# Kernel optimization log

Hardware: AMD Instinct MI355X
Metric: run time of the kernel (lower is better)

The kernel has to match this reference:

```python
import jax, jax.numpy as jnp
import numpy as np

N_NODES = 65536
N_EDGES = 1048576
IN_F = 128
HID_F = 128
OUT_F = 128


def setup_inputs() -> dict:
    key = jax.random.key(0)
    ks = jax.random.split(key, 8)
    feat = jax.random.normal(ks[0], (N_NODES, IN_F), dtype=jnp.float32)
    eweight = jax.random.uniform(ks[1], (N_EDGES, 1), dtype=jnp.float32)
    W1 = jax.random.normal(ks[2], (IN_F, HID_F), dtype=jnp.float32) * (1.0 / np.sqrt(IN_F))
    b1 = jnp.zeros((HID_F,), dtype=jnp.float32)
    W2 = jax.random.normal(ks[3], (HID_F, OUT_F), dtype=jnp.float32) * (1.0 / np.sqrt(HID_F))
    b2 = jnp.zeros((OUT_F,), dtype=jnp.float32)
    src = jax.random.randint(ks[4], (N_EDGES,), 0, N_NODES, dtype=jnp.int32)
    dst = jax.random.randint(ks[5], (N_EDGES,), 0, N_NODES, dtype=jnp.int32)
    return {"feat": feat, "eweight": eweight, "W1": W1, "b1": b1,
            "W2": W2, "b2": b2, "src": src, "dst": dst}


def _degrees(src, dst, n_nodes):
    ones = jnp.ones(src.shape[0], dtype=jnp.float32)
    deg_out = jax.ops.segment_sum(ones, src, num_segments=n_nodes)
    deg_in = jax.ops.segment_sum(ones, dst, num_segments=n_nodes)
    # DGL GraphConv clamps degree to min 1 before norm='both'
    return jnp.clip(deg_out, 1.0, None), jnp.clip(deg_in, 1.0, None)


def _graph_conv(feat, W, b, src, dst, out_norm, in_norm, n_nodes):
    # DGL GraphConv, norm='both': D_out^{-1/2} x -> x W -> spmm sum -> D_in^{-1/2} -> + b
    h = feat * out_norm[:, None]
    h = h @ W
    agg = jax.ops.segment_sum(h[src], dst, num_segments=n_nodes)
    return agg * in_norm[:, None] + b


def reference(feat, eweight, W1, b1, W2, b2, src, dst):
    n = feat.shape[0]
    deg_out, deg_in = _degrees(src, dst, n)
    out_norm = jax.lax.rsqrt(deg_out)
    in_norm = jax.lax.rsqrt(deg_in)
    h = _graph_conv(feat, W1, b1, src, dst, out_norm, in_norm, n)
    h = jax.nn.relu(h)
    h = _graph_conv(h, W2, b2, src, dst, out_norm, in_norm, n)
    # final update_all: u_mul_e + sum (eweight given)
    msg = h[src] * eweight  # [E, OUT_F]
    return jax.ops.segment_sum(msg, dst, num_segments=n)
```

## Files before the change

kernel.cpp:

```cpp
#include <hip/hip_runtime.h>

#define F 128
#define NBA 512
#define NBS 128
#define COARSE 256
#define CAP_BIN 4864
#define CAP_CSR 5632

typedef unsigned int uint;
typedef unsigned short ushort;
typedef unsigned char uchar;
typedef __attribute__((ext_vector_type(8))) short short8;
typedef __attribute__((ext_vector_type(8))) unsigned short ushort8;
typedef __attribute__((ext_vector_type(4))) float floatx4;

__device__ __forceinline__ ushort f2bf(float f) {
  uint u = __float_as_uint(f);
  u += 0x7fffu + ((u >> 16) & 1u);
  return (ushort)(u >> 16);
}

__global__ __launch_bounds__(256) void w_prep(const float* __restrict__ W1,
                                              const float* __restrict__ W2,
                                              ushort* __restrict__ W1t,
                                              ushort* __restrict__ W2t) {
  int b = blockIdx.x;
  const float* W = (b < 64) ? W1 : W2;
  ushort* Wt = (b < 64) ? W1t : W2t;
  int idx = (b & 63) * 256 + threadIdx.x;
  int k = idx >> 7, n = idx & 127;
  Wt[n * F + k] = f2bf(W[idx]);
}

__global__ __launch_bounds__(256) void bin_edges(
    const int* __restrict__ src, const int* __restrict__ dst,
    const float* __restrict__ ew, int E,
    int* __restrict__ cursorD, int* __restrict__ cursorS,
    uint2* __restrict__ slotD, uchar* __restrict__ srcF) {
  __shared__ int cnt[4][COARSE];
  __shared__ int base[COARSE];
  bool isD = blockIdx.x < NBA;
  int blk = isD ? blockIdx.x : blockIdx.x - NBA;
  int nblk = isD ? NBA : NBS;
  const int* key = isD ? dst : src;
  int* cursor = isD ? cursorD : cursorS;
  int wave = threadIdx.x >> 6;
  for (int i = threadIdx.x; i < 4 * COARSE; i += 256) ((int*)cnt)[i] = 0;
  __syncthreads();
  int chunk = (E + nblk - 1) / nblk;
  int s0 = blk * chunk, s1 = min(E, s0 + chunk);
  for (int i = s0 + threadIdx.x; i < s1; i += 256)
    atomicAdd(&cnt[wave][key[i] >> 8], 1);
  __syncthreads();
  if (threadIdx.x < COARSE) {
    int b = threadIdx.x;
    int tot = cnt[0][b] + cnt[1][b] + cnt[2][b] + cnt[3][b];
    base[b] = tot ? atomicAdd(&cursor[b], tot) : 0;
    cnt[0][b] = 0;
  }
  __syncthreads();
  if (isD) {
    for (int i = s0 + threadIdx.x; i < s1; i += 256) {
      int d = dst[i];
      int bin = d >> 8;
      int p = base[bin] + atomicAdd(&cnt[0][bin], 1);
      if (p < CAP_BIN) {
        uint2 v;
        v.x = (uint)(src[i] & 0xffff) | ((uint)f2bf(ew[i]) << 16);
        v.y = (uint)(d & 255);
        slotD[(size_t)bin * CAP_BIN + p] = v;
      }
    }
  } else {
    for (int i = s0 + threadIdx.x; i < s1; i += 256) {
      int s = src[i];
      int bin = s >> 8;
      int p = base[bin] + atomicAdd(&cnt[0][bin], 1);
      if (p < CAP_BIN) srcF[(size_t)bin * CAP_BIN + p] = (uchar)(s & 255);
    }
  }
}

__global__ __launch_bounds__(1024) void bucket_csr(
    const uint2* __restrict__ slotD, const int* __restrict__ cursorD,
    int2* __restrict__ rowRange, float* __restrict__ inNorm, uint* __restrict__ csr,
    const uchar* __restrict__ srcF, const int* __restrict__ cursorS,
    float* __restrict__ outNorm) {
  __shared__ int hist[256], base[256], cur[256];
  int t = threadIdx.x;
  if (blockIdx.x >= COARSE) {
    int b = blockIdx.x - COARSE;
    int lo = b * CAP_BIN;
    int cntS = min(cursorS[b], CAP_BIN);
    if (t < 256) hist[t] = 0;
    __syncthreads();
    for (int i = lo + t; i < lo + cntS; i += 1024)
      atomicAdd(&hist[srcF[i]], 1);
    __syncthreads();
    if (t < 256) outNorm[b * 256 + t] = rsqrtf((float)max(hist[t], 1));
    return;
  }
  int b = blockIdx.x;
  int lo = b * CAP_BIN;
  int cntD = min(cursorD[b], CAP_BIN);
  int hi = lo + cntD;
  if (t < 256) hist[t] = 0;
  __syncthreads();
  for (int i = lo + t; i < hi; i += 1024)
    atomicAdd(&hist[slotD[i].y], 1);
  __syncthreads();
  if (t < 256) base[t] = (hist[t] + 3) & ~3;
  __syncthreads();
  for (int off = 1; off < 256; off <<= 1) {
    int x = 0;
    if (t < 256 && t >= off) x = base[t - off];
    __syncthreads();
    if (t < 256) base[t] += x;
    __syncthreads();
  }
  if (t < 256) {
    int v = hist[t];
    int sz4 = (v + 3) & ~3;
    int st = b * CAP_CSR + base[t] - sz4;
    base[t] = st;
    cur[t] = 0;
    int node = b * 256 + t;
    rowRange[node] = make_int2(st, v);
    inNorm[node] = rsqrtf((float)max(v, 1));
  }
  __syncthreads();
  for (int i = lo + t; i < hi; i += 1024) {
    uint2 v = slotD[i];
    int fine = v.y;
    int p = base[fine] + atomicAdd(&cur[fine], 1);
    csr[p] = v.x;
  }
}


template <bool BF16IN>
__global__ __launch_bounds__(256) void gemm_mfma(
    const void* __restrict__ Xv, const float* __restrict__ scale,
    const ushort* __restrict__ Wt, ushort* __restrict__ Y) {
  __shared__ ushort sA[128 * 136];
  __shared__ ushort sB[128 * 136];
  int t = threadIdx.x;
  int row0 = blockIdx.x * 128;

  {
    int r = t >> 1, hf = t & 1;
    ushort* ap = sA + r * 136 + hf * 64;
    if (BF16IN) {
      const ushort* xp = (const ushort*)Xv + (size_t)(row0 + r) * F + hf * 64;
#pragma unroll
      for (int j = 0; j < 8; ++j)
        *(ushort8*)(ap + j * 8) = *(const ushort8*)(xp + j * 8);
    } else {
      const float* xp = (const float*)Xv + (size_t)(row0 + r) * F + hf * 64;
      float s = scale[row0 + r];
#pragma unroll
      for (int j = 0; j < 8; ++j) {
        float4 v0 = *(const float4*)(xp + j * 8);
        float4 v1 = *(const float4*)(xp + j * 8 + 4);
        ushort8 o;
        o[0] = f2bf(v0.x * s); o[1] = f2bf(v0.y * s); o[2] = f2bf(v0.z * s); o[3] = f2bf(v0.w * s);
        o[4] = f2bf(v1.x * s); o[5] = f2bf(v1.y * s); o[6] = f2bf(v1.z * s); o[7] = f2bf(v1.w * s);
        *(ushort8*)(ap + j * 8) = o;
      }
    }
  }
  {
    int n = t >> 1, hf = t & 1;
    const ushort* wp = Wt + n * F + hf * 64;
    ushort* bp = sB + n * 136 + hf * 64;
#pragma unroll
    for (int j = 0; j < 8; ++j)
      *(ushort8*)(bp + j * 8) = *(const ushort8*)(wp + j * 8);
  }
  __syncthreads();

  int lane = t & 63, wave = t >> 6;
  int quad = lane >> 4, l16 = lane & 15;
  int mrow0 = wave * 32;

  floatx4 acc[2][8];
#pragma unroll
  for (int a = 0; a < 2; ++a)
#pragma unroll
    for (int c = 0; c < 8; ++c) acc[a][c] = (floatx4){0.f, 0.f, 0.f, 0.f};

#pragma unroll
  for (int kc = 0; kc < 128; kc += 32) {
    short8 afrag[2], bfrag[8];
#pragma unroll
    for (int a = 0; a < 2; ++a)
      afrag[a] = *(const short8*)(sA + (mrow0 + a * 16 + l16) * 136 + kc + quad * 8);
#pragma unroll
    for (int c = 0; c < 8; ++c)
      bfrag[c] = *(const short8*)(sB + (c * 16 + l16) * 136 + kc + quad * 8);
#pragma unroll
    for (int a = 0; a < 2; ++a)
#pragma unroll
      for (int c = 0; c < 8; ++c)
        acc[a][c] = __builtin_amdgcn_mfma_f32_16x16x32_bf16(afrag[a], bfrag[c], acc[a][c], 0, 0, 0);
  }

#pragma unroll
  for (int a = 0; a < 2; ++a)
#pragma unroll
    for (int c = 0; c < 8; ++c)
#pragma unroll
      for (int r = 0; r < 4; ++r) {
        int row = row0 + mrow0 + a * 16 + quad * 4 + r;
        int col = c * 16 + l16;
        Y[(size_t)row * F + col] = f2bf(acc[a][c][r]);
      }
}


template <bool EW, bool NB, bool RELU, bool PS, bool OUT_BF16>
__global__ __launch_bounds__(256) void spmm(
    const ushort* __restrict__ hb, const int2* __restrict__ rowRange,
    const uint* __restrict__ csr, const float* __restrict__ inNorm,
    const float* __restrict__ bias, const float* __restrict__ postScale,
    void* __restrict__ outv) {
  int node = blockIdx.x * 4 + (threadIdx.x >> 6);
  int lane = threadIdx.x & 63;
  int2 rr = rowRange[node];
  int base = rr.x, len = rr.y;

  float ax0 = 0.f, ay0 = 0.f, ax1 = 0.f, ay1 = 0.f;
  float ax2 = 0.f, ay2 = 0.f, ax3 = 0.f, ay3 = 0.f;
  int i = 0;
  for (; i + 8 <= len; i += 8) {
    uint4 c0 = *(const uint4*)(csr + base + i);
    uint4 c1 = *(const uint4*)(csr + base + i + 4);
    uint e0 = c0.x, e1 = c0.y, e2 = c0.z, e3 = c0.w;
    uint e4 = c1.x, e5 = c1.y, e6 = c1.z, e7 = c1.w;
    uint w0 = *((const uint*)(hb + ((size_t)(e0 & 0xffffu) << 7)) + lane);
    uint w1 = *((const uint*)(hb + ((size_t)(e1 & 0xffffu) << 7)) + lane);
    uint w2 = *((const uint*)(hb + ((size_t)(e2 & 0xffffu) << 7)) + lane);
    uint w3 = *((const uint*)(hb + ((size_t)(e3 & 0xffffu) << 7)) + lane);
    uint w4 = *((const uint*)(hb + ((size_t)(e4 & 0xffffu) << 7)) + lane);
    uint w5 = *((const uint*)(hb + ((size_t)(e5 & 0xffffu) << 7)) + lane);
    uint w6 = *((const uint*)(hb + ((size_t)(e6 & 0xffffu) << 7)) + lane);
    uint w7 = *((const uint*)(hb + ((size_t)(e7 & 0xffffu) << 7)) + lane);
    if (EW) {
      float q0 = __uint_as_float(e0 & 0xffff0000u), q1 = __uint_as_float(e1 & 0xffff0000u);
      float q2 = __uint_as_float(e2 & 0xffff0000u), q3 = __uint_as_float(e3 & 0xffff0000u);
      float q4 = __uint_as_float(e4 & 0xffff0000u), q5 = __uint_as_float(e5 & 0xffff0000u);
      float q6 = __uint_as_float(e6 & 0xffff0000u), q7 = __uint_as_float(e7 & 0xffff0000u);
      ax0 = fmaf(__uint_as_float(w0 << 16), q0, ax0); ay0 = fmaf(__uint_as_float(w0 & 0xffff0000u), q0, ay0);
      ax1 = fmaf(__uint_as_float(w1 << 16), q1, ax1); ay1 = fmaf(__uint_as_float(w1 & 0xffff0000u), q1, ay1);
      ax2 = fmaf(__uint_as_float(w2 << 16), q2, ax2); ay2 = fmaf(__uint_as_float(w2 & 0xffff0000u), q2, ay2);
      ax3 = fmaf(__uint_as_float(w3 << 16), q3, ax3); ay3 = fmaf(__uint_as_float(w3 & 0xffff0000u), q3, ay3);
      ax0 = fmaf(__uint_as_float(w4 << 16), q4, ax0); ay0 = fmaf(__uint_as_float(w4 & 0xffff0000u), q4, ay0);
      ax1 = fmaf(__uint_as_float(w5 << 16), q5, ax1); ay1 = fmaf(__uint_as_float(w5 & 0xffff0000u), q5, ay1);
      ax2 = fmaf(__uint_as_float(w6 << 16), q6, ax2); ay2 = fmaf(__uint_as_float(w6 & 0xffff0000u), q6, ay2);
      ax3 = fmaf(__uint_as_float(w7 << 16), q7, ax3); ay3 = fmaf(__uint_as_float(w7 & 0xffff0000u), q7, ay3);
    } else {
      ax0 += __uint_as_float(w0 << 16) + __uint_as_float(w4 << 16);
      ay0 += __uint_as_float(w0 & 0xffff0000u) + __uint_as_float(w4 & 0xffff0000u);
      ax1 += __uint_as_float(w1 << 16) + __uint_as_float(w5 << 16);
      ay1 += __uint_as_float(w1 & 0xffff0000u) + __uint_as_float(w5 & 0xffff0000u);
      ax2 += __uint_as_float(w2 << 16) + __uint_as_float(w6 << 16);
      ay2 += __uint_as_float(w2 & 0xffff0000u) + __uint_as_float(w6 & 0xffff0000u);
      ax3 += __uint_as_float(w3 << 16) + __uint_as_float(w7 << 16);
      ay3 += __uint_as_float(w3 & 0xffff0000u) + __uint_as_float(w7 & 0xffff0000u);
    }
  }
  if (i + 4 <= len) {
    uint4 c = *(const uint4*)(csr + base + i);
    uint e0 = c.x, e1 = c.y, e2 = c.z, e3 = c.w;
    uint w0 = *((const uint*)(hb + ((size_t)(e0 & 0xffffu) << 7)) + lane);
    uint w1 = *((const uint*)(hb + ((size_t)(e1 & 0xffffu) << 7)) + lane);
    uint w2 = *((const uint*)(hb + ((size_t)(e2 & 0xffffu) << 7)) + lane);
    uint w3 = *((const uint*)(hb + ((size_t)(e3 & 0xffffu) << 7)) + lane);
    float q0 = EW ? __uint_as_float(e0 & 0xffff0000u) : 1.f;
    float q1 = EW ? __uint_as_float(e1 & 0xffff0000u) : 1.f;
    float q2 = EW ? __uint_as_float(e2 & 0xffff0000u) : 1.f;
    float q3 = EW ? __uint_as_float(e3 & 0xffff0000u) : 1.f;
    ax0 = fmaf(__uint_as_float(w0 << 16), q0, ax0); ay0 = fmaf(__uint_as_float(w0 & 0xffff0000u), q0, ay0);
    ax1 = fmaf(__uint_as_float(w1 << 16), q1, ax1); ay1 = fmaf(__uint_as_float(w1 & 0xffff0000u), q1, ay1);
    ax2 = fmaf(__uint_as_float(w2 << 16), q2, ax2); ay2 = fmaf(__uint_as_float(w2 & 0xffff0000u), q2, ay2);
    ax3 = fmaf(__uint_as_float(w3 << 16), q3, ax3); ay3 = fmaf(__uint_as_float(w3 & 0xffff0000u), q3, ay3);
    i += 4;
  }
  int r = len - i;
  if (r > 0) {
    uint4 c = *(const uint4*)(csr + base + i);
    uint ee[4] = {c.x, c.y, c.z, c.w};
#pragma unroll
    for (int j = 0; j < 3; ++j) {
      if (j < r) {
        uint wj = *((const uint*)(hb + ((size_t)(ee[j] & 0xffffu) << 7)) + lane);
        float q = EW ? __uint_as_float(ee[j] & 0xffff0000u) : 1.f;
        if (j == 0) { ax0 = fmaf(__uint_as_float(wj << 16), q, ax0); ay0 = fmaf(__uint_as_float(wj & 0xffff0000u), q, ay0); }
        if (j == 1) { ax1 = fmaf(__uint_as_float(wj << 16), q, ax1); ay1 = fmaf(__uint_as_float(wj & 0xffff0000u), q, ay1); }
        if (j == 2) { ax2 = fmaf(__uint_as_float(wj << 16), q, ax2); ay2 = fmaf(__uint_as_float(wj & 0xffff0000u), q, ay2); }
      }
    }
  }
  float rx = (ax0 + ax1) + (ax2 + ax3);
  float ry = (ay0 + ay1) + (ay2 + ay3);
  if (NB) {
    float sc = inNorm[node];
    float2 b = *((const float2*)bias + lane);
    rx = fmaf(rx, sc, b.x);
    ry = fmaf(ry, sc, b.y);
    if (RELU) { rx = fmaxf(rx, 0.f); ry = fmaxf(ry, 0.f); }
    if (PS) { float o = postScale[node]; rx *= o; ry *= o; }
  }
  if (OUT_BF16) {
    uint p = ((uint)f2bf(ry) << 16) | (uint)f2bf(rx);
    *((uint*)outv + ((size_t)node << 6) + lane) = p;
  } else {
    float2 rv = {rx, ry};
    *((float2*)outv + ((size_t)node << 6) + lane) = rv;
  }
}


extern "C" void kernel_launch(void* const* d_in, const int* in_sizes, int n_in,
                              void* d_out, int out_size, void* d_ws, size_t ws_size,
                              hipStream_t stream) {
  const float* feat = (const float*)d_in[0];
  const float* ew   = (const float*)d_in[1];
  const float* W1   = (const float*)d_in[2];
  const float* b1   = (const float*)d_in[3];
  const float* W2   = (const float*)d_in[4];
  const float* b2   = (const float*)d_in[5];
  const int*   src  = (const int*)d_in[6];
  const int*   dst  = (const int*)d_in[7];
  const int N = in_sizes[0] / F;
  const int E = in_sizes[6];
  float* out = (float*)d_out;

  char* ws = (char*)d_ws;
  size_t off = 0;
  auto alloc = [&](size_t bytes) {
    void* p = ws + off;
    off += (bytes + 255) & ~(size_t)255;
    return p;
  };
  int2*   rowRange = (int2*)alloc((size_t)N * 8);
  float*  inNorm   = (float*)alloc((size_t)N * 4);
  float*  outNorm  = (float*)alloc((size_t)N * 4);
  ushort* W1t      = (ushort*)alloc((size_t)F * F * 2);
  ushort* W2t      = (ushort*)alloc((size_t)F * F * 2);
  int*    cursorD  = (int*)alloc(COARSE * 4);
  int*    cursorS  = (int*)alloc(COARSE * 4);
  uint*   csr      = (uint*)alloc((size_t)COARSE * CAP_CSR * 4);
  ushort* bufAb    = (ushort*)alloc((size_t)N * F * 2);
  ushort* bufBb    = (ushort*)alloc((size_t)N * F * 2);
  ushort* bufCb    = (ushort*)alloc((size_t)N * F * 2);
  if (off > ws_size) return;

  uint2* slotD;
  uchar* srcF;
  {
    char* tp = (char*)bufBb;
    size_t toff = 0;
    auto talloc = [&](size_t bytes) {
      void* p = tp + toff;
      toff += (bytes + 255) & ~(size_t)255;
      return p;
    };
    slotD = (uint2*)talloc((size_t)COARSE * CAP_BIN * 8);
    srcF  = (uchar*)talloc((size_t)COARSE * CAP_BIN);
  }

  hipMemsetAsync(cursorD, 0, 2 * COARSE * 4, stream);
  w_prep<<<128, 256, 0, stream>>>(W1, W2, W1t, W2t);
  bin_edges<<<NBA + NBS, 256, 0, stream>>>(src, dst, ew, E, cursorD, cursorS, slotD, srcF);
  bucket_csr<<<2 * COARSE, 1024, 0, stream>>>(slotD, cursorD, rowRange, inNorm, csr,
                                              srcF, cursorS, outNorm);

  gemm_mfma<false><<<N / 128, 256, 0, stream>>>(feat, outNorm, W1t, bufAb);
  spmm<false, true, true, true, true><<<N / 4, 256, 0, stream>>>(
      bufAb, rowRange, csr, inNorm, b1, outNorm, bufBb);
  gemm_mfma<true><<<N / 128, 256, 0, stream>>>(bufBb, nullptr, W2t, bufAb);
  spmm<false, true, false, false, true><<<N / 4, 256, 0, stream>>>(
      bufAb, rowRange, csr, inNorm, b2, nullptr, bufCb);
  spmm<true, false, false, false, false><<<N / 4, 256, 0, stream>>>(
      bufCb, rowRange, csr, nullptr, nullptr, nullptr, out);
}
```

Measured before the change: 281.8 us.

## Split SpMM wave into half-waves gathering two edges with 8-byte loads

The SpMM kernel now has each half of a 64-lane wave gather a different neighbor row. Each lane loads 8 bytes (four bf16 features), and the two halves are combined with a cross-half shuffle before the epilogue. This halves the number of gather load instructions per edge and widens each memory access, at the cost of a shuffle reduction and only half the lanes doing the stores. Separately, the binning kernel now keeps a per-wave prefix offset per bin so scatter atomics are spread over four shared counters instead of one, which reduces LDS atomic contention.

```diff
diff --git a/kernel.cpp b/kernel.cpp
--- a/kernel.cpp
+++ b/kernel.cpp
@@ -38,7 +38,6 @@
     int* __restrict__ cursorD, int* __restrict__ cursorS,
     uint2* __restrict__ slotD, uchar* __restrict__ srcF) {
   __shared__ int cnt[4][COARSE];
-  __shared__ int base[COARSE];
   bool isD = blockIdx.x < NBA;
   int blk = isD ? blockIdx.x : blockIdx.x - NBA;
   int nblk = isD ? NBA : NBS;
@@ -54,16 +53,20 @@
   __syncthreads();
   if (threadIdx.x < COARSE) {
     int b = threadIdx.x;
-    int tot = cnt[0][b] + cnt[1][b] + cnt[2][b] + cnt[3][b];
-    base[b] = tot ? atomicAdd(&cursor[b], tot) : 0;
-    cnt[0][b] = 0;
+    int c0 = cnt[0][b], c1 = cnt[1][b], c2 = cnt[2][b], c3 = cnt[3][b];
+    int tot = c0 + c1 + c2 + c3;
+    int base = tot ? atomicAdd(&cursor[b], tot) : 0;
+    cnt[0][b] = base;
+    cnt[1][b] = base + c0;
+    cnt[2][b] = base + c0 + c1;
+    cnt[3][b] = base + c0 + c1 + c2;
   }
   __syncthreads();
   if (isD) {
     for (int i = s0 + threadIdx.x; i < s1; i += 256) {
       int d = dst[i];
       int bin = d >> 8;
-      int p = base[bin] + atomicAdd(&cnt[0][bin], 1);
+      int p = atomicAdd(&cnt[wave][bin], 1);
       if (p < CAP_BIN) {
         uint2 v;
         v.x = (uint)(src[i] & 0xffff) | ((uint)f2bf(ew[i]) << 16);
@@ -75,7 +78,7 @@
     for (int i = s0 + threadIdx.x; i < s1; i += 256) {
       int s = src[i];
       int bin = s >> 8;
-      int p = base[bin] + atomicAdd(&cnt[0][bin], 1);
+      int p = atomicAdd(&cnt[wave][bin], 1);
       if (p < CAP_BIN) srcF[(size_t)bin * CAP_BIN + p] = (uchar)(s & 255);
     }
   }
@@ -137,7 +140,6 @@
   }
 }
 
-
 template <bool BF16IN>
 __global__ __launch_bounds__(256) void gemm_mfma(
     const void* __restrict__ Xv, const float* __restrict__ scale,
@@ -226,97 +228,95 @@
     void* __restrict__ outv) {
   int node = blockIdx.x * 4 + (threadIdx.x >> 6);
   int lane = threadIdx.x & 63;
+  int half = lane >> 5;
+  int l32 = lane & 31;
   int2 rr = rowRange[node];
   int base = rr.x, len = rr.y;
 
-  float ax0 = 0.f, ay0 = 0.f, ax1 = 0.f, ay1 = 0.f;
-  float ax2 = 0.f, ay2 = 0.f, ax3 = 0.f, ay3 = 0.f;
+  float a0 = 0.f, a1 = 0.f, a2 = 0.f, a3 = 0.f;
+  float b0 = 0.f, b1v = 0.f, b2v = 0.f, b3 = 0.f;
+
+#define PAIR(elo, ehi, A0, A1, A2, A3)                                          \
+  {                                                                             \
+    uint es = half ? (ehi) : (elo);                                             \
+    uint2 w = *(const uint2*)(hb + ((size_t)(es & 0xffffu) << 7) + l32 * 4);    \
+    float q = EW ? __uint_as_float(es & 0xffff0000u) : 1.f;                     \
+    A0 = fmaf(__uint_as_float(w.x << 16), q, A0);                               \
+    A1 = fmaf(__uint_as_float(w.x & 0xffff0000u), q, A1);                       \
+    A2 = fmaf(__uint_as_float(w.y << 16), q, A2);                               \
+    A3 = fmaf(__uint_as_float(w.y & 0xffff0000u), q, A3);                       \
+  }
+
   int i = 0;
   for (; i + 8 <= len; i += 8) {
     uint4 c0 = *(const uint4*)(csr + base + i);
     uint4 c1 = *(const uint4*)(csr + base + i + 4);
-    uint e0 = c0.x, e1 = c0.y, e2 = c0.z, e3 = c0.w;
-    uint e4 = c1.x, e5 = c1.y, e6 = c1.z, e7 = c1.w;
-    uint w0 = *((const uint*)(hb + ((size_t)(e0 & 0xffffu) << 7)) + lane);
-    uint w1 = *((const uint*)(hb + ((size_t)(e1 & 0xffffu) << 7)) + lane);
-    uint w2 = *((const uint*)(hb + ((size_t)(e2 & 0xffffu) << 7)) + lane);
-    uint w3 = *((const uint*)(hb + ((size_t)(e3 & 0xffffu) << 7)) + lane);
-    uint w4 = *((const uint*)(hb + ((size_t)(e4 & 0xffffu) << 7)) + lane);
-    uint w5 = *((const uint*)(hb + ((size_t)(e5 & 0xffffu) << 7)) + lane);
-    uint w6 = *((const uint*)(hb + ((size_t)(e6 & 0xffffu) << 7)) + lane);
-    uint w7 = *((const uint*)(hb + ((size_t)(e7 & 0xffffu) << 7)) + lane);
-    if (EW) {
-      float q0 = __uint_as_float(e0 & 0xffff0000u), q1 = __uint_as_float(e1 & 0xffff0000u);
-      float q2 = __uint_as_float(e2 & 0xffff0000u), q3 = __uint_as_float(e3 & 0xffff0000u);
-      float q4 = __uint_as_float(e4 & 0xffff0000u), q5 = __uint_as_float(e5 & 0xffff0000u);
-      float q6 = __uint_as_float(e6 & 0xffff0000u), q7 = __uint_as_float(e7 & 0xffff0000u);
-      ax0 = fmaf(__uint_as_float(w0 << 16), q0, ax0); ay0 = fmaf(__uint_as_float(w0 & 0xffff0000u), q0, ay0);
-      ax1 = fmaf(__uint_as_float(w1 << 16), q1, ax1); ay1 = fmaf(__uint_as_float(w1 & 0xffff0000u), q1, ay1);
-      ax2 = fmaf(__uint_as_float(w2 << 16), q2, ax2); ay2 = fmaf(__uint_as_float(w2 & 0xffff0000u), q2, ay2);
-      ax3 = fmaf(__uint_as_float(w3 << 16), q3, ax3); ay3 = fmaf(__uint_as_float(w3 & 0xffff0000u), q3, ay3);
-      ax0 = fmaf(__uint_as_float(w4 << 16), q4, ax0); ay0 = fmaf(__uint_as_float(w4 & 0xffff0000u), q4, ay0);
-      ax1 = fmaf(__uint_as_float(w5 << 16), q5, ax1); ay1 = fmaf(__uint_as_float(w5 & 0xffff0000u), q5, ay1);
-      ax2 = fmaf(__uint_as_float(w6 << 16), q6, ax2); ay2 = fmaf(__uint_as_float(w6 & 0xffff0000u), q6, ay2);
-      ax3 = fmaf(__uint_as_float(w7 << 16), q7, ax3); ay3 = fmaf(__uint_as_float(w7 & 0xffff0000u), q7, ay3);
-    } else {
-      ax0 += __uint_as_float(w0 << 16) + __uint_as_float(w4 << 16);
-      ay0 += __uint_as_float(w0 & 0xffff0000u) + __uint_as_float(w4 & 0xffff0000u);
-      ax1 += __uint_as_float(w1 << 16) + __uint_as_float(w5 << 16);
-      ay1 += __uint_as_float(w1 & 0xffff0000u) + __uint_as_float(w5 & 0xffff0000u);
-      ax2 += __uint_as_float(w2 << 16) + __uint_as_float(w6 << 16);
-      ay2 += __uint_as_float(w2 & 0xffff0000u) + __uint_as_float(w6 & 0xffff0000u);
-      ax3 += __uint_as_float(w3 << 16) + __uint_as_float(w7 << 16);
-      ay3 += __uint_as_float(w3 & 0xffff0000u) + __uint_as_float(w7 & 0xffff0000u);
-    }
+    PAIR(c0.x, c0.y, a0, a1, a2, a3)
+    PAIR(c0.z, c0.w, b0, b1v, b2v, b3)
+    PAIR(c1.x, c1.y, a0, a1, a2, a3)
+    PAIR(c1.z, c1.w, b0, b1v, b2v, b3)
   }
   if (i + 4 <= len) {
     uint4 c = *(const uint4*)(csr + base + i);
-    uint e0 = c.x, e1 = c.y, e2 = c.z, e3 = c.w;
-    uint w0 = *((const uint*)(hb + ((size_t)(e0 & 0xffffu) << 7)) + lane);
-    uint w1 = *((const uint*)(hb + ((size_t)(e1 & 0xffffu) << 7)) + lane);
-    uint w2 = *((const uint*)(hb + ((size_t)(e2 & 0xffffu) << 7)) + lane);
-    uint w3 = *((const uint*)(hb + ((size_t)(e3 & 0xffffu) << 7)) + lane);
-    float q0 = EW ? __uint_as_float(e0 & 0xffff0000u) : 1.f;
-    float q1 = EW ? __uint_as_float(e1 & 0xffff0000u) : 1.f;
-    float q2 = EW ? __uint_as_float(e2 & 0xffff0000u) : 1.f;
-    float q3 = EW ? __uint_as_float(e3 & 0xffff0000u) : 1.f;
-    ax0 = fmaf(__uint_as_float(w0 << 16), q0, ax0); ay0 = fmaf(__uint_as_float(w0 & 0xffff0000u), q0, ay0);
-    ax1 = fmaf(__uint_as_float(w1 << 16), q1, ax1); ay1 = fmaf(__uint_as_float(w1 & 0xffff0000u), q1, ay1);
-    ax2 = fmaf(__uint_as_float(w2 << 16), q2, ax2); ay2 = fmaf(__uint_as_float(w2 & 0xffff0000u), q2, ay2);
-    ax3 = fmaf(__uint_as_float(w3 << 16), q3, ax3); ay3 = fmaf(__uint_as_float(w3 & 0xffff0000u), q3, ay3);
+    PAIR(c.x, c.y, a0, a1, a2, a3)
+    PAIR(c.z, c.w, b0, b1v, b2v, b3)
     i += 4;
   }
   int r = len - i;
   if (r > 0) {
     uint4 c = *(const uint4*)(csr + base + i);
-    uint ee[4] = {c.x, c.y, c.z, c.w};
-#pragma unroll
-    for (int j = 0; j < 3; ++j) {
-      if (j < r) {
-        uint wj = *((const uint*)(hb + ((size_t)(ee[j] & 0xffffu) << 7)) + lane);
-        float q = EW ? __uint_as_float(ee[j] & 0xffff0000u) : 1.f;
-        if (j == 0) { ax0 = fmaf(__uint_as_float(wj << 16), q, ax0); ay0 = fmaf(__uint_as_float(wj & 0xffff0000u), q, ay0); }
-        if (j == 1) { ax1 = fmaf(__uint_as_float(wj << 16), q, ax1); ay1 = fmaf(__uint_as_float(wj & 0xffff0000u), q, ay1); }
-        if (j == 2) { ax2 = fmaf(__uint_as_float(wj << 16), q, ax2); ay2 = fmaf(__uint_as_float(wj & 0xffff0000u), q, ay2); }
-      }
-    }
-  }
-  float rx = (ax0 + ax1) + (ax2 + ax3);
-  float ry = (ay0 + ay1) + (ay2 + ay3);
+    {
+      uint es = half ? c.y : c.x;
+      int k = i + half;
+      uint2 w = *(const uint2*)(hb + ((size_t)(es & 0xffffu) << 7) + l32 * 4);
+      float q = EW ? __uint_as_float(es & 0xffff0000u) : 1.f;
+      q = (k < len) ? q : 0.f;
+      a0 = fmaf(__uint_as_float(w.x << 16), q, a0);
+      a1 = fmaf(__uint_as_float(w.x & 0xffff0000u), q, a1);
+      a2 = fmaf(__uint_as_float(w.y << 16), q, a2);
+      a3 = fmaf(__uint_as_float(w.y & 0xffff0000u), q, a3);
+    }
+    if (r > 2) {
+      uint es = half ? c.w : c.z;
+      int k = i + 2 + half;
+      uint2 w = *(const uint2*)(hb + ((size_t)(es & 0xffffu) << 7) + l32 * 4);
+      float q = EW ? __uint_as_float(es & 0xffff0000u) : 1.f;
+      q = (k < len) ? q : 0.f;
+      b0 = fmaf(__uint_as_float(w.x << 16), q, b0);
+      b1v = fmaf(__uint_as_float(w.x & 0xffff0000u), q, b1v);
+      b2v = fmaf(__uint_as_float(w.y << 16), q, b2v);
+      b3 = fmaf(__uint_as_float(w.y & 0xffff0000u), q, b3);
+    }
+  }
+#undef PAIR
+  float r0 = a0 + b0, r1 = a1 + b1v, r2 = a2 + b2v, r3 = a3 + b3;
+  r0 += __shfl_xor(r0, 32, 64);
+  r1 += __shfl_xor(r1, 32, 64);
+  r2 += __shfl_xor(r2, 32, 64);
+  r3 += __shfl_xor(r3, 32, 64);
   if (NB) {
     float sc = inNorm[node];
-    float2 b = *((const float2*)bias + lane);
-    rx = fmaf(rx, sc, b.x);
-    ry = fmaf(ry, sc, b.y);
-    if (RELU) { rx = fmaxf(rx, 0.f); ry = fmaxf(ry, 0.f); }
-    if (PS) { float o = postScale[node]; rx *= o; ry *= o; }
-  }
-  if (OUT_BF16) {
-    uint p = ((uint)f2bf(ry) << 16) | (uint)f2bf(rx);
-    *((uint*)outv + ((size_t)node << 6) + lane) = p;
-  } else {
-    float2 rv = {rx, ry};
-    *((float2*)outv + ((size_t)node << 6) + lane) = rv;
+    float4 bv = *((const float4*)bias + l32);
+    r0 = fmaf(r0, sc, bv.x);
+    r1 = fmaf(r1, sc, bv.y);
+    r2 = fmaf(r2, sc, bv.z);
+    r3 = fmaf(r3, sc, bv.w);
+    if (RELU) {
+      r0 = fmaxf(r0, 0.f); r1 = fmaxf(r1, 0.f);
+      r2 = fmaxf(r2, 0.f); r3 = fmaxf(r3, 0.f);
+    }
+    if (PS) { float o = postScale[node]; r0 *= o; r1 *= o; r2 *= o; r3 *= o; }
+  }
+  if (half == 0) {
+    if (OUT_BF16) {
+      uint2 p;
+      p.x = ((uint)f2bf(r1) << 16) | (uint)f2bf(r0);
+      p.y = ((uint)f2bf(r3) << 16) | (uint)f2bf(r2);
+      *((uint2*)outv + ((size_t)node << 5) + l32) = p;
+    } else {
+      float4 rv = {r0, r1, r2, r3};
+      *((float4*)outv + ((size_t)node << 5) + l32) = rv;
+    }
   }
 }
 
```

New measurement: 285.2 us. Within noise of the previous version (+1.2%).
